# Optimization experiments

Hardware: AMD Instinct MI355X
Metric: run time of the kernel (lower is better)

## Reference

```python
import jax, jax.numpy as jnp
import numpy as np

N_NODES = 20000
N_ATTRS = 5000
IN_FEATURES = 512
OUT_FEATURES = 128
ALPHA = 0.2  # LeakyReLU negative slope
NEG_INF = -9e15


def setup_inputs() -> dict:
    key = jax.random.key(0)
    k1, k2, k3, k4, k5 = jax.random.split(key, 5)
    node_embedding = jax.random.normal(k1, (N_NODES, IN_FEATURES), dtype=jnp.float32)
    attr_embedding = jax.random.normal(k2, (N_ATTRS, IN_FEATURES), dtype=jnp.float32)
    feat_mat = jax.random.randint(k3, (N_NODES, N_ATTRS), 0, 2, dtype=jnp.int32)
    # xavier_uniform with gain=1.414 (as in torch init)
    gain = 1.414
    lim_W = gain * np.sqrt(6.0 / (IN_FEATURES + OUT_FEATURES))
    W = jax.random.uniform(k4, (IN_FEATURES, OUT_FEATURES), minval=-lim_W, maxval=lim_W, dtype=jnp.float32)
    lim_a = gain * np.sqrt(6.0 / (2 * OUT_FEATURES + 1))
    a = jax.random.uniform(k5, (2 * OUT_FEATURES, 1), minval=-lim_a, maxval=lim_a, dtype=jnp.float32)
    return {"node_embedding": node_embedding, "attr_embedding": attr_embedding,
            "feat_mat": feat_mat, "W": W, "a": a}


def reference(node_embedding, attr_embedding, feat_mat, W, a):
    # Linear projections
    node_h = node_embedding @ W            # [N, F]
    attr_h = attr_embedding @ W            # [M, F]
    # Additive attention scores: e[i,j] = leakyrelu(a1.node_h[i] + a2.attr_h[j])
    wh1 = node_h @ a[:OUT_FEATURES, :]     # [N, 1]
    wh2 = attr_h @ a[OUT_FEATURES:, :]     # [M, 1]
    e = jax.nn.leaky_relu(wh1 + wh2.T, negative_slope=ALPHA)  # [N, M]
    # Mask where there is no node-attribute link, then softmax over attrs
    attention = jnp.where(feat_mat > 0, e, NEG_INF)
    attention = jax.nn.softmax(attention, axis=1)
    # (dropout is identity in eval mode)
    h_prime = attention @ attr_h           # [N, F]
    return jax.nn.elu(h_prime)             # concat=True branch
```

## Files before the change

### kernel.cpp

```cpp
#include <hip/hip_runtime.h>

#define N_NODES 20000
#define N_ATTRS 5000
#define IN_F    512
#define OUT_F   128
#define NK      160
#define NSS     80
#define WH2_PAD 5376
#define NEGBIG  -1e30f
#define LOG2E   1.4426950408889634f

typedef _Float16 f16x8 __attribute__((ext_vector_type(8)));
typedef float    f32x4 __attribute__((ext_vector_type(4)));
typedef int      i32x4 __attribute__((ext_vector_type(4)));

__device__ __forceinline__ float fast_exp2(float x) {
    return __builtin_amdgcn_exp2f(x);
}

__device__ __forceinline__ void async16(void* lds_dst, const void* gsrc) {
    __builtin_amdgcn_global_load_lds(
        (const __attribute__((address_space(1))) unsigned int*)gsrc,
        (__attribute__((address_space(3))) unsigned int*)lds_dst, 16, 0, 0);
}

__global__ __launch_bounds__(256) void prep_kernel(
    const float* __restrict__ W, const float* __restrict__ a,
    float* __restrict__ Wa1, float* __restrict__ Wa2, _Float16* __restrict__ Wp) {
    int gt = blockIdx.x * blockDim.x + threadIdx.x;
    if (gt < IN_F) {
        int k = gt;
        float s1 = 0.f, s2 = 0.f;
        for (int f = 0; f < OUT_F; ++f) {
            float w = W[k * OUT_F + f];
            s1 += w * a[f];
            s2 += w * a[OUT_F + f];
        }
        Wa1[k] = s1 * LOG2E;
        Wa2[k] = s2 * LOG2E;
    }
    for (int idx = gt; idx < IN_F * OUT_F; idx += gridDim.x * blockDim.x) {
        int j    = idx & 7;
        int lane = (idx >> 3) & 63;
        int nb   = (idx >> 9) & 7;
        int kb   = idx >> 12;
        int k = kb * 32 + (lane >> 4) * 8 + j;
        int n = nb * 16 + (lane & 15);
        Wp[idx] = (_Float16)W[k * OUT_F + n];
    }
}

__global__ __launch_bounds__(256) void wh_kernel(
    const float* __restrict__ node_emb, const float* __restrict__ attr_emb,
    const float* __restrict__ Wa1, const float* __restrict__ Wa2,
    float* __restrict__ wh1, float* __restrict__ wh2) {
    int wave = threadIdx.x >> 6, lane = threadIdx.x & 63;
    int r = blockIdx.x * 4 + wave;
    const float* src;
    const float* vec;
    float* dst;
    if (r < N_NODES) {
        src = node_emb + (size_t)r * IN_F; vec = Wa1; dst = wh1 + r;
    } else {
        int r2 = r - N_NODES;
        src = attr_emb + (size_t)r2 * IN_F; vec = Wa2; dst = wh2 + r2;
    }
    float4 ra = *reinterpret_cast<const float4*>(src + lane * 8);
    float4 rb = *reinterpret_cast<const float4*>(src + lane * 8 + 4);
    const float* vp = vec + lane * 8;
    float s = ra.x * vp[0] + ra.y * vp[1] + ra.z * vp[2] + ra.w * vp[3]
            + rb.x * vp[4] + rb.y * vp[5] + rb.z * vp[6] + rb.w * vp[7];
#pragma unroll
    for (int off = 1; off < 64; off <<= 1) s += __shfl_xor(s, off, 64);
    if (lane == 0) *dst = s;
}

__global__ __launch_bounds__(256) void max_kernel(
    float* __restrict__ wh2, float* __restrict__ maxp) {
    __shared__ float red[4];
    int t = threadIdx.x;
    float m = -1e30f;
    for (int j = t; j < N_ATTRS; j += 256) m = fmaxf(m, wh2[j]);
    for (int j = N_ATTRS + t; j < WH2_PAD; j += 256) wh2[j] = NEGBIG;
#pragma unroll
    for (int off = 1; off < 64; off <<= 1) m = fmaxf(m, __shfl_xor(m, off, 64));
    int wave = t >> 6, lane = t & 63;
    if (lane == 0) red[wave] = m;
    __syncthreads();
    if (t == 0) *maxp = fmaxf(fmaxf(red[0], red[1]), fmaxf(red[2], red[3]));
}

__global__ __launch_bounds__(64) void attr_h_kernel(
    const float* __restrict__ attr_emb, const _Float16* __restrict__ Wp,
    _Float16* __restrict__ Vp) {
    int lane = threadIdx.x & 63;
    int m = lane & 15, quad = lane >> 4;
    int j0 = blockIdx.x * 16;
    int j = j0 + m;
    bool valid = j < N_ATTRS;
    f32x4 acc[8];
#pragma unroll
    for (int nb = 0; nb < 8; ++nb)
#pragma unroll
        for (int t = 0; t < 4; ++t) acc[nb][t] = 0.f;
    const float* arow = attr_emb + (size_t)j * IN_F;
    for (int kk = 0; kk < IN_F / 32; ++kk) {
        f16x8 afrag;
        if (valid) {
            float4 ra = *reinterpret_cast<const float4*>(arow + kk * 32 + quad * 8);
            float4 rb = *reinterpret_cast<const float4*>(arow + kk * 32 + quad * 8 + 4);
            afrag[0] = (_Float16)ra.x; afrag[1] = (_Float16)ra.y;
            afrag[2] = (_Float16)ra.z; afrag[3] = (_Float16)ra.w;
            afrag[4] = (_Float16)rb.x; afrag[5] = (_Float16)rb.y;
            afrag[6] = (_Float16)rb.z; afrag[7] = (_Float16)rb.w;
        } else {
#pragma unroll
            for (int t = 0; t < 8; ++t) afrag[t] = (_Float16)0.f;
        }
        const _Float16* wbase = Wp + (size_t)(kk * 8) * 64 * 8;
#pragma unroll
        for (int nb = 0; nb < 8; ++nb) {
            f16x8 bfrag;
            __builtin_memcpy(&bfrag, wbase + (nb * 64 + lane) * 8, 16);
            acc[nb] = __builtin_amdgcn_mfma_f32_16x16x32_f16(afrag, bfrag, acc[nb], 0, 0, 0);
        }
    }
#pragma unroll
    for (int nb = 0; nb < 8; ++nb) {
#pragma unroll
        for (int reg = 0; reg < 4; ++reg) {
            int jr = j0 + quad * 4 + reg;
            int n = nb * 16 + m;
            float v = (jr < N_ATTRS) ? acc[nb][reg] : 0.f;
            size_t idx = ((size_t)((jr >> 5) * 8 + nb) * 64 +
                          (((jr >> 3) & 3) * 16 + m)) * 8 + (jr & 7);
            Vp[idx] = (_Float16)v;
        }
    }
}

__global__ __launch_bounds__(256, 4) void attn_kernel(
    const int* __restrict__ feat, const float* __restrict__ wh1,
    const float* __restrict__ wh2, const float* __restrict__ maxwh2,
    const _Float16* __restrict__ Vp, float* __restrict__ out) {
    __shared__ __align__(16) char lds[16896];
    __shared__ float rsums[32];

    int wave = threadIdx.x >> 6, lane = threadIdx.x & 63;
    int m = lane & 15, quad = lane >> 4;
    int i0 = blockIdx.x * 32;
    int rg = (wave >> 1) * 16;
    int half = wave & 1;

    float wh1i = wh1[i0 + rg + m];
    float emax = wh1i + maxwh2[0];
    float Mi = fmaxf(emax, 0.2f * emax) - 12.f;

    f32x4 acc[8];
#pragma unroll
    for (int nb = 0; nb < 8; ++nb)
#pragma unroll
        for (int t = 0; t < 4; ++t) acc[nb][t] = 0.f;
    float s = 0.f;

    char* fbuf0 = lds;
    char* wbuf0 = lds + 16384;

    const char* featb = (const char*)feat;
    size_t frow_off = (size_t)(i0 + rg + m) * N_ATTRS * 4;

    auto stage = [&](int ss, int b) {
        int kbase = (2 * ss + half) * 32;
        char* fdst = fbuf0 + b * 8192 + wave * 2048;
#pragma unroll
        for (int h = 0; h < 2; ++h) {
            int a = kbase + quad * 8 + h * 4;
            a = min(a, N_ATTRS - 4);
            async16(fdst + h * 1024, featb + frow_off + (size_t)a * 4);
        }
        if (wave == 0 && lane < 16)
            async16(wbuf0 + b * 256, (const char*)(wh2 + ss * 64) + lane * 16);
    };

    stage(0, 0);
    __syncthreads();

    for (int ss = 0; ss < NSS; ++ss) {
        int cur = ss & 1;

        f16x8 bf[8];
        const _Float16* vb = Vp + (size_t)(2 * ss + half) * 4096 + lane * 8;
#pragma unroll
        for (int nb = 0; nb < 8; ++nb)
            bf[nb] = *reinterpret_cast<const f16x8*>(vb + nb * 512);
        __builtin_amdgcn_sched_barrier(0);

        if (ss + 1 < NSS) stage(ss + 1, cur ^ 1);

        char* wb = wbuf0 + cur * 256 + half * 128 + quad * 32;
        float4 wva = *reinterpret_cast<const float4*>(wb);
        float4 wvb = *reinterpret_cast<const float4*>(wb + 16);
        char* fb = fbuf0 + cur * 8192 + wave * 2048 + lane * 16;
        i32x4 fA = *reinterpret_cast<const i32x4*>(fb);
        i32x4 fB = *reinterpret_cast<const i32x4*>(fb + 1024);

        int   fi[8] = {fA.x, fA.y, fA.z, fA.w, fB.x, fB.y, fB.z, fB.w};
        float wv[8] = {wva.x, wva.y, wva.z, wva.w, wvb.x, wvb.y, wvb.z, wvb.w};
        f16x8 afrag;
#pragma unroll
        for (int t = 0; t < 8; ++t) {
            float e = wh1i + wv[t];
            float l = fmaxf(e, 0.2f * e);
            float p = fast_exp2(l - Mi);
            p = (fi[t] > 0) ? p : 0.f;
            _Float16 ph = (_Float16)p;
            s += (float)ph;
            afrag[t] = ph;
        }

#pragma unroll
        for (int nb = 0; nb < 8; ++nb)
            acc[nb] = __builtin_amdgcn_mfma_f32_16x16x32_f16(afrag, bf[nb], acc[nb], 0, 0, 0);

        __syncthreads();
    }

    s += __shfl_xor(s, 16, 64);
    s += __shfl_xor(s, 32, 64);

    float* accp = (float*)lds;
    if (half == 0) {
#pragma unroll
        for (int nb = 0; nb < 8; ++nb)
#pragma unroll
            for (int reg = 0; reg < 4; ++reg)
                accp[(rg + quad * 4 + reg) * 128 + nb * 16 + m] = acc[nb][reg];
        if (lane < 16) rsums[rg + lane] = s;
    }
    __syncthreads();
    if (half == 1) {
#pragma unroll
        for (int nb = 0; nb < 8; ++nb)
#pragma unroll
            for (int reg = 0; reg < 4; ++reg)
                accp[(rg + quad * 4 + reg) * 128 + nb * 16 + m] += acc[nb][reg];
        if (lane < 16) rsums[rg + lane] += s;
    }
    __syncthreads();

    for (int o = threadIdx.x; o < 32 * 128; o += 256) {
        int lr = o >> 7, n = o & 127;
        float v = accp[lr * 128 + n];
        float rs = rsums[lr];
        rs = (rs > 0.f) ? rs : 1.f;
        float h = v / rs;
        float ov = (h > 0.f) ? h : (fast_exp2(h * LOG2E) - 1.f);
        out[(size_t)(i0 + lr) * OUT_F + n] = ov;
    }
}

extern "C" void kernel_launch(void* const* d_in, const int* in_sizes, int n_in,
                              void* d_out, int out_size, void* d_ws, size_t ws_size,
                              hipStream_t stream) {
    const float* node_emb = (const float*)d_in[0];
    const float* attr_emb = (const float*)d_in[1];
    const int*   feat     = (const int*)d_in[2];
    const float* W        = (const float*)d_in[3];
    const float* a        = (const float*)d_in[4];
    float*       out      = (float*)d_out;

    char* ws = (char*)d_ws;
    float*    Wa1 = (float*)(ws + 0);
    float*    Wa2 = (float*)(ws + 4096);
    float*    wh1 = (float*)(ws + 8192);
    float*    wh2 = (float*)(ws + 90112);
    float*    mx  = (float*)(ws + 111616);
    _Float16* Wp  = (_Float16*)(ws + 131072);
    _Float16* Vp  = (_Float16*)(ws + 262144);

    prep_kernel<<<64, 256, 0, stream>>>(W, a, Wa1, Wa2, Wp);
    wh_kernel<<<6250, 256, 0, stream>>>(node_emb, attr_emb, Wa1, Wa2, wh1, wh2);
    max_kernel<<<1, 256, 0, stream>>>(wh2, mx);
    attr_h_kernel<<<320, 64, 0, stream>>>(attr_emb, Wp, Vp);
    attn_kernel<<<625, 256, 0, stream>>>(feat, wh1, wh2, mx, Vp, out);
}
```

Before: 661.6 us.

## Pack feat mask into bitmask kernel and preload it into LDS for attention

Adds a pack_kernel that reads the int32 feature matrix once and writes a per-row bitmask in a swizzled layout. The attention kernel then loads each block's whole bitmask into LDS up front, which removes the per-step staging of feat and wh2 and the per-iteration __syncthreads. The V-fragment and wh2 loads are software-pipelined across two register buffers, with launch bounds lowered to 2 blocks per SIMD. The trade-offs are an extra kernel launch plus a separate full pass over the 400 MB feat matrix, and higher register use.

```diff
diff --git a/kernel.cpp b/kernel.cpp
--- a/kernel.cpp
+++ b/kernel.cpp
@@ -139,11 +139,40 @@
     }
 }
 
-__global__ __launch_bounds__(256, 4) void attn_kernel(
-    const int* __restrict__ feat, const float* __restrict__ wh1,
+__global__ __launch_bounds__(256) void pack_kernel(
+    const int* __restrict__ feat, unsigned* __restrict__ fmask) {
+    int u = blockIdx.x * 256 + threadIdx.x;
+    int row = u / 160;
+    int kk  = u - row * 160;
+    int ko  = (kk & ~31) | ((kk & 31) ^ ((2 * (row & 15)) & 31));
+    unsigned bits = 0;
+    if (ko < 156) {
+        const int* p = feat + (size_t)row * N_ATTRS + ko * 32;
+#pragma unroll
+        for (int q = 0; q < 8; ++q) {
+            i32x4 v = *reinterpret_cast<const i32x4*>(p + q * 4);
+            unsigned b = (v.x > 0 ? 1u : 0u) | (v.y > 0 ? 2u : 0u)
+                       | (v.z > 0 ? 4u : 0u) | (v.w > 0 ? 8u : 0u);
+            bits |= b << (q * 4);
+        }
+    } else if (ko == 156) {
+        const int* p = feat + (size_t)row * N_ATTRS + 4992;
+#pragma unroll
+        for (int q = 0; q < 2; ++q) {
+            i32x4 v = *reinterpret_cast<const i32x4*>(p + q * 4);
+            unsigned b = (v.x > 0 ? 1u : 0u) | (v.y > 0 ? 2u : 0u)
+                       | (v.z > 0 ? 4u : 0u) | (v.w > 0 ? 8u : 0u);
+            bits |= b << (q * 4);
+        }
+    }
+    fmask[u] = bits;
+}
+
+__global__ __launch_bounds__(256, 2) void attn_kernel(
+    const unsigned* __restrict__ fmask, const float* __restrict__ wh1,
     const float* __restrict__ wh2, const float* __restrict__ maxwh2,
     const _Float16* __restrict__ Vp, float* __restrict__ out) {
-    __shared__ __align__(16) char lds[16896];
+    __shared__ __align__(16) char lds[20480];
     __shared__ float rsums[32];
 
     int wave = threadIdx.x >> 6, lane = threadIdx.x & 63;
@@ -152,6 +181,15 @@
     int rg = (wave >> 1) * 16;
     int half = wave & 1;
 
+    {
+        const char* src = (const char*)(fmask + (size_t)i0 * 160);
+#pragma unroll
+        for (int q = 0; q < 5; ++q) {
+            int off = q * 4096 + wave * 1024;
+            async16(lds + off, src + off + lane * 16);
+        }
+    }
+
     float wh1i = wh1[i0 + rg + m];
     float emax = wh1i + maxwh2[0];
     float Mi = fmaxf(emax, 0.2f * emax) - 12.f;
@@ -163,70 +201,58 @@
         for (int t = 0; t < 4; ++t) acc[nb][t] = 0.f;
     float s = 0.f;
 
-    char* fbuf0 = lds;
-    char* wbuf0 = lds + 16384;
-
-    const char* featb = (const char*)feat;
-    size_t frow_off = (size_t)(i0 + rg + m) * N_ATTRS * 4;
-
-    auto stage = [&](int ss, int b) {
-        int kbase = (2 * ss + half) * 32;
-        char* fdst = fbuf0 + b * 8192 + wave * 2048;
-#pragma unroll
-        for (int h = 0; h < 2; ++h) {
-            int a = kbase + quad * 8 + h * 4;
-            a = min(a, N_ATTRS - 4);
-            async16(fdst + h * 1024, featb + frow_off + (size_t)a * 4);
-        }
-        if (wave == 0 && lane < 16)
-            async16(wbuf0 + b * 256, (const char*)(wh2 + ss * 64) + lane * 16);
-    };
-
-    stage(0, 0);
-    __syncthreads();
-
-    for (int ss = 0; ss < NSS; ++ss) {
-        int cur = ss & 1;
-
-        f16x8 bf[8];
+    const unsigned* fml = (const unsigned*)lds;
+    int swz = (2 * m) & 31;
+    int fbase = (rg + m) * 160;
+
+    f16x8  bf0[8], bf1[8];
+    float4 w0a, w0b, w1a, w1b;
+    auto loadV = [&](int ss, f16x8* bf, float4& wa, float4& wb) {
         const _Float16* vb = Vp + (size_t)(2 * ss + half) * 4096 + lane * 8;
 #pragma unroll
         for (int nb = 0; nb < 8; ++nb)
             bf[nb] = *reinterpret_cast<const f16x8*>(vb + nb * 512);
-        __builtin_amdgcn_sched_barrier(0);
-
-        if (ss + 1 < NSS) stage(ss + 1, cur ^ 1);
-
-        char* wb = wbuf0 + cur * 256 + half * 128 + quad * 32;
-        float4 wva = *reinterpret_cast<const float4*>(wb);
-        float4 wvb = *reinterpret_cast<const float4*>(wb + 16);
-        char* fb = fbuf0 + cur * 8192 + wave * 2048 + lane * 16;
-        i32x4 fA = *reinterpret_cast<const i32x4*>(fb);
-        i32x4 fB = *reinterpret_cast<const i32x4*>(fb + 1024);
-
-        int   fi[8] = {fA.x, fA.y, fA.z, fA.w, fB.x, fB.y, fB.z, fB.w};
-        float wv[8] = {wva.x, wva.y, wva.z, wva.w, wvb.x, wvb.y, wvb.z, wvb.w};
+        const float* wp = wh2 + ss * 64 + half * 32 + quad * 8;
+        wa = *reinterpret_cast<const float4*>(wp);
+        wb = *reinterpret_cast<const float4*>(wp + 4);
+    };
+
+    auto compute = [&](int ss, const f16x8* bf, float4 wa, float4 wb) {
+        int k = 2 * ss + half;
+        int kk = (k & ~31) | ((k & 31) ^ swz);
+        unsigned fm = fml[fbase + kk] >> (quad * 8);
+        float wv[8] = {wa.x, wa.y, wa.z, wa.w, wb.x, wb.y, wb.z, wb.w};
         f16x8 afrag;
 #pragma unroll
         for (int t = 0; t < 8; ++t) {
             float e = wh1i + wv[t];
             float l = fmaxf(e, 0.2f * e);
             float p = fast_exp2(l - Mi);
-            p = (fi[t] > 0) ? p : 0.f;
+            p = (fm & (1u << t)) ? p : 0.f;
             _Float16 ph = (_Float16)p;
             s += (float)ph;
             afrag[t] = ph;
         }
-
 #pragma unroll
         for (int nb = 0; nb < 8; ++nb)
             acc[nb] = __builtin_amdgcn_mfma_f32_16x16x32_f16(afrag, bf[nb], acc[nb], 0, 0, 0);
-
-        __syncthreads();
+    };
+
+    loadV(0, bf0, w0a, w0b);
+    __syncthreads();
+
+    for (int ss = 0; ss < NSS; ss += 2) {
+        loadV(ss + 1, bf1, w1a, w1b);
+        compute(ss, bf0, w0a, w0b);
+        int kn = (ss + 2 < NSS) ? ss + 2 : NSS - 1;
+        loadV(kn, bf0, w0a, w0b);
+        compute(ss + 1, bf1, w1a, w1b);
     }
 
     s += __shfl_xor(s, 16, 64);
     s += __shfl_xor(s, 32, 64);
+
+    __syncthreads();
 
     float* accp = (float*)lds;
     if (half == 0) {
@@ -277,10 +303,12 @@
     float*    mx  = (float*)(ws + 111616);
     _Float16* Wp  = (_Float16*)(ws + 131072);
     _Float16* Vp  = (_Float16*)(ws + 262144);
+    unsigned* fmk = (unsigned*)(ws + 2097152);
 
     prep_kernel<<<64, 256, 0, stream>>>(W, a, Wa1, Wa2, Wp);
     wh_kernel<<<6250, 256, 0, stream>>>(node_emb, attr_emb, Wa1, Wa2, wh1, wh2);
     max_kernel<<<1, 256, 0, stream>>>(wh2, mx);
     attr_h_kernel<<<320, 64, 0, stream>>>(attr_emb, Wp, Vp);
-    attn_kernel<<<625, 256, 0, stream>>>(feat, wh1, wh2, mx, Vp, out);
-}
+    pack_kernel<<<12500, 256, 0, stream>>>(feat, fmk);
+    attn_kernel<<<625, 256, 0, stream>>>(fmk, wh1, wh2, mx, Vp, out);
+}
```

After: 671.7 us. Within noise of the previous version (+1.5%).
